# Kernel tuning notes

Measured on AMD Instinct MI355X. Metric: run time of the kernel, lower is better.

The kernel has to match this reference:

```python
import jax, jax.numpy as jnp
import numpy as np
from jax.scipy.special import logsumexp

T, B, V, E, H, K = 512, 64, 50000, 300, 256, 20


def setup_inputs() -> dict:
    key = jax.random.key(0)
    ks = jax.random.split(key, 12)
    s_e, s_h = 1.0 / np.sqrt(E), 1.0 / np.sqrt(H)
    return {
        "inp": jax.random.randint(ks[0], (T, B), 0, V),
        "labels": jax.random.randint(ks[1], (T, B), 0, K),
        "emb_table": jax.random.normal(ks[2], (V, E), jnp.float32) * 0.1,
        "w_ih": jax.random.uniform(ks[3], (4 * H, E), jnp.float32, -s_h, s_h),
        "w_hh": jax.random.uniform(ks[4], (4 * H, H), jnp.float32, -s_h, s_h),
        "b_ih": jax.random.uniform(ks[5], (4 * H,), jnp.float32, -s_h, s_h),
        "b_hh": jax.random.uniform(ks[6], (4 * H,), jnp.float32, -s_h, s_h),
        "W_lin": jax.random.uniform(ks[7], (K, H), jnp.float32, -s_h, s_h),
        "b_lin": jax.random.uniform(ks[8], (K,), jnp.float32, -s_h, s_h),
        "start_trans": jax.random.uniform(ks[9], (K,), jnp.float32, -0.1, 0.1),
        "end_trans": jax.random.uniform(ks[10], (K,), jnp.float32, -0.1, 0.1),
        "trans": jax.random.uniform(ks[11], (K, K), jnp.float32, -0.1, 0.1),
    }


def _lstm(x, w_ih, w_hh, b_ih, b_hh):
    # x: (T, B, E) -> outputs (T, B, H). PyTorch gate order: i, f, g, o.
    def step(carry, xt):
        h, c = carry
        gates = xt @ w_ih.T + b_ih + h @ w_hh.T + b_hh  # (B, 4H)
        i, f, g, o = jnp.split(gates, 4, axis=-1)
        c = jax.nn.sigmoid(f) * c + jax.nn.sigmoid(i) * jnp.tanh(g)
        h = jax.nn.sigmoid(o) * jnp.tanh(c)
        return (h, c), h
    z = jnp.zeros((x.shape[1], w_hh.shape[1]), x.dtype)
    _, outs = jax.lax.scan(step, (z, z), x)
    return outs


def _crf_nll(emissions, tags, start_trans, end_trans, trans):
    # emissions: (T, B, K), tags: (T, B). Returns -sum(log-likelihood) (torchcrf reduction='sum').
    b_idx = jnp.arange(emissions.shape[1])
    # numerator: score of the gold path
    score0 = start_trans[tags[0]] + emissions[0, b_idx, tags[0]]  # (B,)
    def score_step(s, xs):
        em_t, tag_prev, tag_t = xs
        return s + trans[tag_prev, tag_t] + em_t[b_idx, tag_t], None
    score, _ = jax.lax.scan(score_step, score0, (emissions[1:], tags[:-1], tags[1:]))
    score = score + end_trans[tags[-1]]
    # denominator: forward algorithm (logsumexp DP over tags)
    def fwd_step(alpha, em_t):
        # alpha: (B, K) log-scores over previous tag
        alpha = logsumexp(alpha[:, :, None] + trans[None] + em_t[:, None, :], axis=1)
        return alpha, None
    alpha0 = start_trans[None, :] + emissions[0]
    alpha, _ = jax.lax.scan(fwd_step, alpha0, emissions[1:])
    logZ = logsumexp(alpha + end_trans[None, :], axis=1)  # (B,)
    return -jnp.sum(score - logZ)


def reference(inp, labels, emb_table, w_ih, w_hh, b_ih, b_hh, W_lin, b_lin,
              start_trans, end_trans, trans):
    x = emb_table[inp]                           # (T, B, E); dropout = identity (eval)
    outs = _lstm(x, w_ih, w_hh, b_ih, b_hh)      # (T, B, H)
    emissions = outs @ W_lin.T + b_lin           # (T, B, K)
    return _crf_nll(emissions, labels, start_trans, end_trans, trans)
```

## Files before the change

### kernel.cpp

```cpp
#include <hip/hip_runtime.h>
#include <math.h>

#define T_ 512
#define B_ 64
#define V_ 50000
#define E_ 300
#define H_ 256
#define K_ 20
#define G4 1024
#define LOG2E 1.44269504f
#define LN2 0.69314718f

typedef float f4 __attribute__((ext_vector_type(4)));
typedef int v4i __attribute__((ext_vector_type(4)));
typedef int v8i __attribute__((ext_vector_type(8)));
typedef short bf16x8 __attribute__((ext_vector_type(8)));
typedef _Float16 h2_t __attribute__((ext_vector_type(2)));
union U32H2 { unsigned u; h2_t h; };
__device__ __forceinline__ h2_t u2h(unsigned u) { U32H2 x; x.u = u; return x.h; }
__device__ __forceinline__ unsigned h2u(h2_t h) { U32H2 x; x.h = h; return x.u; }

__device__ __forceinline__ float rcpf(float x) { return __builtin_amdgcn_rcpf(x); }
__device__ __forceinline__ float exp2f_(float x) { return __builtin_amdgcn_exp2f(x); }

__device__ __forceinline__ unsigned short f32_bf16(float x) {
  union { float f; unsigned u; } v; v.f = x;
  v.u += 0x7FFFu + ((v.u >> 16) & 1u);
  return (unsigned short)(v.u >> 16);
}

__device__ __forceinline__ unsigned f32_e2m1(float x) {
  float a = fabsf(x);
  unsigned m = (a >= 0.25f) + (a >= 0.75f) + (a >= 1.25f) + (a >= 1.75f)
             + (a >= 2.5f)  + (a >= 3.5f)  + (a >= 5.f);
  return (x < 0.f ? 8u : 0u) | m;
}

__device__ __forceinline__ void block_sync_lds() {
  asm volatile("s_waitcnt lgkmcnt(0)" ::: "memory");
  __builtin_amdgcn_s_barrier();
}

#define WSCALE4 64.f
#define HSCALE4 4.f
#define DESCALE4 (LOG2E / (WSCALE4 * HSCALE4))
#define SC1 0x7F7F7F7F

__global__ void prep_kernel(const int* __restrict__ inp,
                            const float* __restrict__ emb,
                            const float* __restrict__ w_ih, const float* __restrict__ w_hh,
                            const float* __restrict__ b_ih, const float* __restrict__ b_hh,
                            unsigned short* __restrict__ Xh, unsigned short* __restrict__ wA,
                            unsigned char* __restrict__ W4,
                            float* __restrict__ b_comb, float* __restrict__ out) {
  int tid = blockIdx.x * blockDim.x + threadIdx.x;
  int nth = gridDim.x * blockDim.x;
  for (int i = tid; i < 32768 * 80; i += nth) {
    int row = i / 80, c4 = i % 80, k = c4 * 4;
    ushort4 st;
    if (c4 < 75) {
      int tok = inp[row];
      float4 v = *(const float4*)(emb + (long)tok * E_ + k);
      st.x = f32_bf16(v.x); st.y = f32_bf16(v.y); st.z = f32_bf16(v.z); st.w = f32_bf16(v.w);
    } else {
      st.x = st.y = st.z = st.w = 0;
    }
    *(ushort4*)(Xh + (long)row * 320 + k) = st;
  }
  for (int i = tid; i < 10 * 4 * 1024 * 8; i += nth) {
    int j = i & 7, n = (i >> 3) & 1023, q = (i >> 13) & 3, c = i >> 15;
    int k = c * 32 + q * 8 + j;
    wA[i] = (k < E_) ? f32_bf16(w_ih[n * E_ + k]) : 0;
  }
  for (int i = tid; i < G4 * (H_ / 2); i += nth) {
    int row = i >> 7, kb = i & 127;
    unsigned lo = f32_e2m1(w_hh[row * H_ + 2 * kb]     * WSCALE4);
    unsigned hi = f32_e2m1(w_hh[row * H_ + 2 * kb + 1] * WSCALE4);
    W4[i] = (unsigned char)(lo | (hi << 4));
  }
  for (int i = tid; i < G4; i += nth) b_comb[i] = b_ih[i] + b_hh[i];
  if (tid == 0) out[0] = 0.f;
}

__global__ __launch_bounds__(256) void kernelA(const unsigned short* __restrict__ Xh,
                                               const unsigned short* __restrict__ wA,
                                               const float* __restrict__ b_comb,
                                               _Float16* __restrict__ g_in) {
  __shared__ __align__(16) unsigned short xs[32 * 328];
  int bm = blockIdx.x >> 2, bn = blockIdx.x & 3;
  int tid = threadIdx.x;
  for (int i = tid; i < 32 * 40; i += 256) {
    int r = i / 40, c = i % 40;
    *(uint4*)&xs[r * 328 + c * 8] = *(const uint4*)(Xh + (long)(bm * 32 + r) * 320 + c * 8);
  }
  __syncthreads();
  int lane = tid & 63, w = tid >> 6, col = lane & 15, quad = lane >> 4;
  int nbase = bn * 256 + w * 64;
  f4 acc[2][4];
#pragma unroll
  for (int mt = 0; mt < 2; mt++)
#pragma unroll
    for (int nt = 0; nt < 4; nt++) acc[mt][nt] = (f4){0.f, 0.f, 0.f, 0.f};
#pragma unroll 2
  for (int c = 0; c < 10; c++) {
    bf16x8 a[4], b[2];
#pragma unroll
    for (int nt = 0; nt < 4; nt++)
      a[nt] = *(const bf16x8*)(wA + (((long)c * 4 + quad) * 1024 + nbase + nt * 16 + col) * 8);
#pragma unroll
    for (int mt = 0; mt < 2; mt++)
      b[mt] = *(const bf16x8*)&xs[(mt * 16 + col) * 328 + c * 32 + quad * 8];
#pragma unroll
    for (int mt = 0; mt < 2; mt++)
#pragma unroll
      for (int nt = 0; nt < 4; nt++)
        acc[mt][nt] = __builtin_amdgcn_mfma_f32_16x16x32_bf16(a[nt], b[mt], acc[mt][nt], 0, 0, 0);
  }
#pragma unroll
  for (int mt = 0; mt < 2; mt++) {
    int m = bm * 32 + mt * 16 + col;
#pragma unroll
    for (int nt = 0; nt < 4; nt++) {
      int n = nbase + nt * 16 + quad * 4;
      f4 o = (acc[mt][nt] + *(const f4*)(b_comb + n)) * LOG2E;
      h2_t p0, p1;
      p0.x = (_Float16)o.x; p0.y = (_Float16)o.y;
      p1.x = (_Float16)o.z; p1.y = (_Float16)o.w;
      uint2 st; st.x = h2u(p0); st.y = h2u(p1);
      *(uint2*)(g_in + (long)m * G4 + n) = st;
    }
  }
}

__global__ __launch_bounds__(256, 1) void kernelB(const _Float16* __restrict__ g_in,
                                                  const unsigned char* __restrict__ W4,
                                                  _Float16* __restrict__ houts) {
  int bb = blockIdx.x;
  int tid = threadIdx.x;
  int lane = tid & 63, w = tid >> 6;
  int col = lane & 15, quad = lane >> 4;
  int r = col >> 2;
  int s2 = col & 3;

  __shared__ __align__(16) unsigned char h4[2][144];
  __shared__ __align__(16) _Float16 hlin[2][256];

  for (int i = tid; i < 2 * 144; i += 256) ((unsigned char*)h4)[i] = 0;

  v8i wfv[32];
#pragma unroll
  for (int idx = 0; idx < 32; idx++) {
    int tau = idx >> 3, sp = (idx >> 1) & 3, c = idx & 1;
    const unsigned char* rp = W4 + (unsigned)(256 * tau + 64 * w + 16 * sp + col) * 128 + 64 * c + 16 * quad;
    v4i q0 = *(const v4i*)rp;
    wfv[idx] = __builtin_shufflevector(q0, q0, 0, 1, 2, 3, -1, -1, -1, -1);
  }

  f4 zero4 = {0.f, 0.f, 0.f, 0.f};
  asm volatile("" : "+v"(zero4));

  int myk = 64 * w + 16 * s2 + 4 * quad + r;
  int mybyte = myk >> 1;
  const unsigned char* bp0 = &h4[0][16 * quad];
  const unsigned char* bp1 = &h4[1][16 * quad];
  const _Float16* gbase = g_in + (long)bb * G4 + myk;

  float cst = 0.f;
  float gi_ = (float)gbase[0];
  float gf_ = (float)gbase[256];
  float gg_ = (float)gbase[512];
  float go_ = (float)gbase[768];
  const _Float16* gp = gbase + (long)B_ * G4;

  __syncthreads();

#pragma unroll 2
  for (int t = 0; t < T_; t++) {
    const unsigned char* bptr = (t & 1) ? bp1 : bp0;
    v4i q0 = *(const v4i*)(bptr);
    v4i q1 = *(const v4i*)(bptr + 64);
    v8i b0 = __builtin_shufflevector(q0, q0, 0, 1, 2, 3, -1, -1, -1, -1);
    v8i b1 = __builtin_shufflevector(q1, q1, 0, 1, 2, 3, -1, -1, -1, -1);

    f4 acc[16];
#pragma unroll
    for (int i = 0; i < 16; i++)
      acc[i] = __builtin_amdgcn_mfma_scale_f32_16x16x128_f8f6f4(wfv[i * 2 + 0], b0, zero4, 4, 4, 0, SC1, 0, SC1);
#pragma unroll
    for (int i = 0; i < 16; i++)
      acc[i] = __builtin_amdgcn_mfma_scale_f32_16x16x128_f8f6f4(wfv[i * 2 + 1], b1, acc[i], 4, 4, 0, SC1, 0, SC1);

    if (t > 0 && lane < 8) {
      int buf = (t - 1) & 1;
      int idx = w * 8 + lane;
      uint4 v = *(const uint4*)&hlin[buf][idx * 8];
      *(uint4*)(houts + ((long)(t - 1) * B_ + bb) * H_ + idx * 8) = v;
    }
    _Float16 nh0 = gp[0];
    _Float16 nh1 = gp[256];
    _Float16 nh2 = gp[512];
    _Float16 nh3 = gp[768];
    gp += (long)B_ * G4;

    int s2b0 = s2 & 1, s2b1 = s2 >> 1;
    f4 e0a = s2b0 ? acc[1] : acc[0];
    f4 e0b = s2b0 ? acc[3] : acc[2];
    f4 g0v = s2b1 ? e0b : e0a;
    f4 e1a = s2b0 ? acc[5] : acc[4];
    f4 e1b = s2b0 ? acc[7] : acc[6];
    f4 g1v = s2b1 ? e1b : e1a;
    f4 e2a = s2b0 ? acc[9] : acc[8];
    f4 e2b = s2b0 ? acc[11] : acc[10];
    f4 g2v = s2b1 ? e2b : e2a;
    f4 e3a = s2b0 ? acc[13] : acc[12];
    f4 e3b = s2b0 ? acc[15] : acc[14];
    f4 g3v = s2b1 ? e3b : e3a;

    float gi = g0v[r] * DESCALE4 + gi_;
    float gf = g1v[r] * DESCALE4 + gf_;
    float gg = g2v[r] * DESCALE4 + gg_;
    float go = g3v[r] * DESCALE4 + go_;
    float si = rcpf(1.f + exp2f_(-gi));
    float sf = rcpf(1.f + exp2f_(-gf));
    float so = rcpf(1.f + exp2f_(-go));
    float tg = 1.f - 2.f * rcpf(1.f + exp2f_(gg + gg));
    cst = sf * cst + si * tg;
    float tc_ = 1.f - 2.f * rcpf(1.f + exp2f_(2.88539008f * cst));
    float h = so * tc_;

    unsigned code = f32_e2m1(h * HSCALE4);
    unsigned pc = (unsigned)__shfl_xor((int)code, 4);
    if (!(myk & 1)) h4[1 - (t & 1)][mybyte] = (unsigned char)(code | (pc << 4));
    hlin[t & 1][myk] = (_Float16)h;

    gi_ = (float)nh0; gf_ = (float)nh1; gg_ = (float)nh2; go_ = (float)nh3;
    block_sync_lds();
  }
  if (lane < 8) {
    int idx = w * 8 + lane;
    uint4 v = *(const uint4*)&hlin[1][idx * 8];
    *(uint4*)(houts + ((long)511 * B_ + bb) * H_ + idx * 8) = v;
  }
}

__global__ __launch_bounds__(256) void kernelC(const _Float16* __restrict__ houts,
                                               const float* __restrict__ W_lin,
                                               const float* __restrict__ b_lin,
                                               float* __restrict__ em) {
  __shared__ float hs[32][260];
  __shared__ float wl[20][260];
  __shared__ float bl[20];
  int bm = blockIdx.x;
  int tid = threadIdx.x;
  for (int i = tid; i < 32 * 64; i += 256) {
    int r = i >> 6, c = i & 63;
    uint2 v = *(const uint2*)(houts + ((long)(bm * 32 + r)) * H_ + c * 4);
    h2_t h0 = u2h(v.x), h1 = u2h(v.y);
    *(float4*)&hs[r][c * 4] = make_float4((float)h0.x, (float)h0.y, (float)h1.x, (float)h1.y);
  }
  for (int i = tid; i < 20 * 64; i += 256) {
    int k = i >> 6, c = i & 63;
    *(float4*)&wl[k][c * 4] = *(const float4*)(W_lin + k * H_ + c * 4);
  }
  if (tid < 20) bl[tid] = b_lin[tid];
  __syncthreads();
  for (int o = tid; o < 32 * 20; o += 256) {
    int r = o / 20, k = o % 20;
    float s = 0.f;
#pragma unroll 4
    for (int i = 0; i < H_; i++) s += hs[r][i] * wl[k][i];
    em[(long)bm * 32 * K_ + o] = s + bl[k];
  }
}

__global__ __launch_bounds__(128) void kernelD(const float* __restrict__ em,
                                               const int* __restrict__ labels,
                                               const float* __restrict__ start_t,
                                               const float* __restrict__ end_t,
                                               const float* __restrict__ trans,
                                               float* __restrict__ out) {
  int b = blockIdx.x;
  int tid = threadIdx.x;
  int lane = tid & 63;
  int wv = tid >> 6;
  if (wv == 0) {
    int k = lane & 31;
    bool vk = (k < K_);
    int kk = vk ? k : 0;
    float E[20];
#pragma unroll
    for (int j = 0; j < 20; j++) E[j] = vk ? __expf(trans[j * 20 + k]) : 0.f;
    float end2 = vk ? end_t[kk] * LOG2E : -1e30f;
    float raw0 = (start_t[kk] + em[b * K_ + kk]) * LOG2E;
    float D2 = __shfl(raw0, 0, 32);
    float a2 = vk ? (raw0 - D2) : -1e30f;
    float C2 = D2;
    float emk = em[(64 + b) * K_ + kk];
    for (int t = 1; t < T_; t++) {
      float em_next = (t < T_ - 1) ? em[((long)(t + 1) * B_ + b) * K_ + kk] : 0.f;
      float e = exp2f_(a2);
      float S0 = 0.f, S1 = 0.f, S2 = 0.f, S3 = 0.f;
#pragma unroll
      for (int j = 0; j < 5; j++) {
        S0 = fmaf(__shfl(e, j, 32),      E[j],      S0);
        S1 = fmaf(__shfl(e, j + 5, 32),  E[j + 5],  S1);
        S2 = fmaf(__shfl(e, j + 10, 32), E[j + 10], S2);
        S3 = fmaf(__shfl(e, j + 15, 32), E[j + 15], S3);
      }
      float S = (S0 + S1) + (S2 + S3);
      float raw = emk * LOG2E + __log2f(S);
      float Dn = __shfl(raw, 0, 32);
      a2 = vk ? (raw - Dn) : -1e30f;
      C2 += Dn;
      emk = em_next;
    }
    float fin = vk ? (a2 + end2) : -1e30f;
    float m = fin;
#pragma unroll
    for (int off = 16; off >= 1; off >>= 1) m = fmaxf(m, __shfl_xor(m, off, 32));
    float e = vk ? exp2f_(fin - m) : 0.f;
#pragma unroll
    for (int off = 16; off >= 1; off >>= 1) e += __shfl_xor(e, off, 32);
    if (lane == 0) atomicAdd(out, LN2 * (C2 + m + __log2f(e)));
  } else {
    int t0 = 8 * lane;
    int tags[9];
#pragma unroll
    for (int i = 0; i < 9; i++) {
      int t = t0 - 1 + i;
      tags[i] = (t >= 0) ? labels[t * B_ + b] : 0;
    }
    float sc = 0.f;
#pragma unroll
    for (int i = 1; i < 9; i++) {
      int t = t0 - 1 + i;
      float v = em[((long)t * B_ + b) * K_ + tags[i]];
      v += (t > 0) ? trans[tags[i - 1] * 20 + tags[i]] : start_t[tags[i]];
      sc += v;
    }
#pragma unroll
    for (int off = 32; off >= 1; off >>= 1) sc += __shfl_xor(sc, off, 64);
    if (lane == 0) {
      sc += end_t[labels[511 * B_ + b]];
      atomicAdd(out, -sc);
    }
  }
}

extern "C" void kernel_launch(void* const* d_in, const int* in_sizes, int n_in,
                              void* d_out, int out_size, void* d_ws, size_t ws_size,
                              hipStream_t stream) {
  const int*   inp     = (const int*)d_in[0];
  const int*   labels  = (const int*)d_in[1];
  const float* emb     = (const float*)d_in[2];
  const float* w_ih    = (const float*)d_in[3];
  const float* w_hh    = (const float*)d_in[4];
  const float* b_ih    = (const float*)d_in[5];
  const float* b_hh    = (const float*)d_in[6];
  const float* W_lin   = (const float*)d_in[7];
  const float* b_lin   = (const float*)d_in[8];
  const float* start_t = (const float*)d_in[9];
  const float* end_t   = (const float*)d_in[10];
  const float* trans   = (const float*)d_in[11];
  float* out = (float*)d_out;
  char* ws = (char*)d_ws;
  (void)ws_size;

  _Float16*       g_in   = (_Float16*)(ws);
  unsigned short* Xh     = (unsigned short*)(ws + 67108864);
  _Float16*       houts  = (_Float16*)(ws + 67108864);
  float*          em     = (float*)(ws + 88080384);
  unsigned short* wA     = (unsigned short*)(ws + 90701824);
  unsigned char*  W4     = (unsigned char*)(ws + 91357184);
  float*          b_comb = (float*)(ws + 91619328);

  prep_kernel<<<2048, 256, 0, stream>>>(inp, emb, w_ih, w_hh, b_ih, b_hh, Xh, wA, W4, b_comb, out);
  kernelA<<<4096, 256, 0, stream>>>(Xh, wA, b_comb, g_in);
  kernelB<<<64, 256, 0, stream>>>(g_in, W4, houts);
  kernelC<<<1024, 256, 0, stream>>>(houts, W_lin, b_lin, em);
  kernelD<<<64, 128, 0, stream>>>(em, labels, start_t, end_t, trans, out);
}
```

Measured before the change: 707.9 us.

## Swap MFMA operand roles so each lane owns one hidden unit directly

Hidden state now goes into the A operand and the weights into the B operand of the scaled fp4 MFMA. The output layout then maps lane to hidden index, so each lane picks element 0 of the accumulators with quad-based selects instead of col-based indexing. Each lane stores its fp16 h straight to global memory, which removes the LDS hlin staging buffer and the deferred vector store. The fp4 packing shuffle changes from xor 4 to xor 1 with a simpler byte address. The risk is that the per-lane 2-byte global stores replace coalesced 16-byte stores inside the serial recurrence loop.

New measurement: 577.0 us. -18.5%, faster.

```diff
diff --git a/kernel.cpp b/kernel.cpp
--- a/kernel.cpp
+++ b/kernel.cpp
@@ -34,6 +34,10 @@
   unsigned m = (a >= 0.25f) + (a >= 0.75f) + (a >= 1.25f) + (a >= 1.75f)
              + (a >= 2.5f)  + (a >= 3.5f)  + (a >= 5.f);
   return (x < 0.f ? 8u : 0u) | m;
+}
+
+__device__ __forceinline__ v8i ext8(v4i x) {
+  return __builtin_shufflevector(x, x, 0, 1, 2, 3, -1, -1, -1, -1);
 }
 
 __device__ __forceinline__ void block_sync_lds() {
@@ -139,31 +143,27 @@
   int tid = threadIdx.x;
   int lane = tid & 63, w = tid >> 6;
   int col = lane & 15, quad = lane >> 4;
-  int r = col >> 2;
-  int s2 = col & 3;
 
   __shared__ __align__(16) unsigned char h4[2][144];
-  __shared__ __align__(16) _Float16 hlin[2][256];
 
   for (int i = tid; i < 2 * 144; i += 256) ((unsigned char*)h4)[i] = 0;
 
-  v8i wfv[32];
+  v4i wf4[32];
 #pragma unroll
   for (int idx = 0; idx < 32; idx++) {
     int tau = idx >> 3, sp = (idx >> 1) & 3, c = idx & 1;
     const unsigned char* rp = W4 + (unsigned)(256 * tau + 64 * w + 16 * sp + col) * 128 + 64 * c + 16 * quad;
-    v4i q0 = *(const v4i*)rp;
-    wfv[idx] = __builtin_shufflevector(q0, q0, 0, 1, 2, 3, -1, -1, -1, -1);
+    wf4[idx] = *(const v4i*)rp;
   }
 
   f4 zero4 = {0.f, 0.f, 0.f, 0.f};
   asm volatile("" : "+v"(zero4));
 
-  int myk = 64 * w + 16 * s2 + 4 * quad + r;
-  int mybyte = myk >> 1;
-  const unsigned char* bp0 = &h4[0][16 * quad];
-  const unsigned char* bp1 = &h4[1][16 * quad];
+  int myk = 64 * w + lane;
+  const unsigned char* ap0 = &h4[0][16 * quad];
+  const unsigned char* ap1 = &h4[1][16 * quad];
   const _Float16* gbase = g_in + (long)bb * G4 + myk;
+  _Float16* hp = houts + (long)bb * H_ + myk;
 
   float cst = 0.f;
   float gi_ = (float)gbase[0];
@@ -172,54 +172,48 @@
   float go_ = (float)gbase[768];
   const _Float16* gp = gbase + (long)B_ * G4;
 
+  bool qb0 = (quad & 1) != 0;
+  bool qb1 = (quad & 2) != 0;
+
   __syncthreads();
 
 #pragma unroll 2
   for (int t = 0; t < T_; t++) {
-    const unsigned char* bptr = (t & 1) ? bp1 : bp0;
-    v4i q0 = *(const v4i*)(bptr);
-    v4i q1 = *(const v4i*)(bptr + 64);
-    v8i b0 = __builtin_shufflevector(q0, q0, 0, 1, 2, 3, -1, -1, -1, -1);
-    v8i b1 = __builtin_shufflevector(q1, q1, 0, 1, 2, 3, -1, -1, -1, -1);
+    const unsigned char* aptr = (t & 1) ? ap1 : ap0;
+    v8i a0 = ext8(*(const v4i*)(aptr));
+    v8i a1 = ext8(*(const v4i*)(aptr + 64));
 
     f4 acc[16];
 #pragma unroll
     for (int i = 0; i < 16; i++)
-      acc[i] = __builtin_amdgcn_mfma_scale_f32_16x16x128_f8f6f4(wfv[i * 2 + 0], b0, zero4, 4, 4, 0, SC1, 0, SC1);
+      acc[i] = __builtin_amdgcn_mfma_scale_f32_16x16x128_f8f6f4(a0, ext8(wf4[i * 2 + 0]), zero4, 4, 4, 0, SC1, 0, SC1);
 #pragma unroll
     for (int i = 0; i < 16; i++)
-      acc[i] = __builtin_amdgcn_mfma_scale_f32_16x16x128_f8f6f4(wfv[i * 2 + 1], b1, acc[i], 4, 4, 0, SC1, 0, SC1);
-
-    if (t > 0 && lane < 8) {
-      int buf = (t - 1) & 1;
-      int idx = w * 8 + lane;
-      uint4 v = *(const uint4*)&hlin[buf][idx * 8];
-      *(uint4*)(houts + ((long)(t - 1) * B_ + bb) * H_ + idx * 8) = v;
-    }
+      acc[i] = __builtin_amdgcn_mfma_scale_f32_16x16x128_f8f6f4(a1, ext8(wf4[i * 2 + 1]), acc[i], 4, 4, 0, SC1, 0, SC1);
+
     _Float16 nh0 = gp[0];
     _Float16 nh1 = gp[256];
     _Float16 nh2 = gp[512];
     _Float16 nh3 = gp[768];
     gp += (long)B_ * G4;
 
-    int s2b0 = s2 & 1, s2b1 = s2 >> 1;
-    f4 e0a = s2b0 ? acc[1] : acc[0];
-    f4 e0b = s2b0 ? acc[3] : acc[2];
-    f4 g0v = s2b1 ? e0b : e0a;
-    f4 e1a = s2b0 ? acc[5] : acc[4];
-    f4 e1b = s2b0 ? acc[7] : acc[6];
-    f4 g1v = s2b1 ? e1b : e1a;
-    f4 e2a = s2b0 ? acc[9] : acc[8];
-    f4 e2b = s2b0 ? acc[11] : acc[10];
-    f4 g2v = s2b1 ? e2b : e2a;
-    f4 e3a = s2b0 ? acc[13] : acc[12];
-    f4 e3b = s2b0 ? acc[15] : acc[14];
-    f4 g3v = s2b1 ? e3b : e3a;
-
-    float gi = g0v[r] * DESCALE4 + gi_;
-    float gf = g1v[r] * DESCALE4 + gf_;
-    float gg = g2v[r] * DESCALE4 + gg_;
-    float go = g3v[r] * DESCALE4 + go_;
+    float t0a = qb0 ? acc[1][0]  : acc[0][0];
+    float t0b = qb0 ? acc[3][0]  : acc[2][0];
+    float gir = qb1 ? t0b : t0a;
+    float t1a = qb0 ? acc[5][0]  : acc[4][0];
+    float t1b = qb0 ? acc[7][0]  : acc[6][0];
+    float gfr = qb1 ? t1b : t1a;
+    float t2a = qb0 ? acc[9][0]  : acc[8][0];
+    float t2b = qb0 ? acc[11][0] : acc[10][0];
+    float ggr = qb1 ? t2b : t2a;
+    float t3a = qb0 ? acc[13][0] : acc[12][0];
+    float t3b = qb0 ? acc[15][0] : acc[14][0];
+    float gor = qb1 ? t3b : t3a;
+
+    float gi = gir * DESCALE4 + gi_;
+    float gf = gfr * DESCALE4 + gf_;
+    float gg = ggr * DESCALE4 + gg_;
+    float go = gor * DESCALE4 + go_;
     float si = rcpf(1.f + exp2f_(-gi));
     float sf = rcpf(1.f + exp2f_(-gf));
     float so = rcpf(1.f + exp2f_(-go));
@@ -229,17 +223,14 @@
     float h = so * tc_;
 
     unsigned code = f32_e2m1(h * HSCALE4);
-    unsigned pc = (unsigned)__shfl_xor((int)code, 4);
-    if (!(myk & 1)) h4[1 - (t & 1)][mybyte] = (unsigned char)(code | (pc << 4));
-    hlin[t & 1][myk] = (_Float16)h;
+    unsigned pc = (unsigned)__shfl_xor((int)code, 1);
+    if (!(lane & 1)) h4[1 - (t & 1)][32 * w + (lane >> 1)] = (unsigned char)(code | (pc << 4));
+
+    *hp = (_Float16)h;
+    hp += (long)B_ * H_;
 
     gi_ = (float)nh0; gf_ = (float)nh1; gg_ = (float)nh2; go_ = (float)nh3;
     block_sync_lds();
-  }
-  if (lane < 8) {
-    int idx = w * 8 + lane;
-    uint4 v = *(const uint4*)&hlin[1][idx * 8];
-    *(uint4*)(houts + ((long)511 * B_ + bb) * H_ + idx * 8) = v;
   }
 }
 
```
